# Optimization experiments

Hardware: AMD Instinct MI355X
Metric: run time of the kernel (lower is better)

## Reference

```python
import jax, jax.numpy as jnp
import numpy as np

B, T, D = 1, 4096, 1024
H, DK, DV, L = 16, 64, 64, 32
ROT_SCALE = 1.0  # rotary_pos_scale default


def _rotate_half(x):
    # '... (j d) -> ... j d' with j=2, then cat((-x2, x1))
    x1, x2 = jnp.split(x, 2, axis=-1)
    return jnp.concatenate((-x2, x1), axis=-1)


def _apply_rope(freqs, x, scale):
    # freqs: [T, L] broadcasts over leading dims of x [..., T, L]
    return x * jnp.cos(freqs) * scale + _rotate_half(x) * jnp.sin(freqs) * scale


def setup_inputs() -> dict:
    key = jax.random.key(0)
    ks = jax.random.split(key, 9)
    q = jax.random.normal(ks[0], (B, T, D), jnp.float32)
    k = jax.random.normal(ks[1], (B, T, D), jnp.float32)
    v = jax.random.normal(ks[2], (B, T, D), jnp.float32)
    mask = jnp.tril(jnp.ones((T, T), dtype=bool))  # causal [T, T]
    rotary_freqs = jax.random.normal(ks[3], (T, L), jnp.float32)
    s = 0.02
    w_q = jax.random.normal(ks[4], (H * DK, D), jnp.float32) * s
    w_k = jax.random.normal(ks[5], (H * DK, D), jnp.float32) * s
    w_v = jax.random.normal(ks[6], (H * DV, D), jnp.float32) * s
    w_o = jax.random.normal(ks[7], (D, H * DV), jnp.float32) * s
    return {"q": q, "k": k, "v": v, "mask": mask, "rotary_freqs": rotary_freqs,
            "w_q": w_q, "w_k": w_k, "w_v": w_v, "w_o": w_o}


def reference(q, k, v, mask, rotary_freqs, w_q, w_k, w_v, w_o):
    # project and split heads: '... T (H k) -> ... H T k'
    def heads(x, w, dh):
        y = jnp.einsum('btd,ed->bte', x, w)
        return y.reshape(B, T, H, dh).transpose(0, 2, 1, 3)  # [B,H,T,dh]

    q_i = heads(q, w_q, DK)
    k_i = heads(k, w_k, DK)
    v_i = heads(v, w_v, DV)

    # rotary pos emb on first L dims of q, k AND v (unusual: v too)
    q_scale, k_scale = ROT_SCALE, ROT_SCALE ** (-1.0)

    def rope(x, scale):
        xl, xr = x[..., :L], x[..., L:]
        return jnp.concatenate((_apply_rope(rotary_freqs, xl, scale), xr), axis=-1)

    q_i = rope(q_i, q_scale)
    k_i = rope(k_i, k_scale)
    v_i = rope(v_i, k_scale)

    s_qk = jnp.einsum('bhik,bhjk->bhij', q_i, k_i) / (DK ** 0.5)
    neg = -jnp.finfo(s_qk.dtype).max
    s_qk = jnp.where(mask, s_qk, neg)  # mask broadcasts [T,T] -> [B,H,T,T]
    attn = jax.nn.softmax(s_qk, axis=-1)
    vals = jnp.einsum('bhij,bhjv->bhiv', attn, v_i)
    vals = vals.transpose(0, 2, 1, 3).reshape(B, T, H * DV)  # '... H T v -> ... T (H v)'
    out = jnp.einsum('bte,oe->bto', vals, w_o)
    return out
```

## Files before the change

### kernel.cpp

```cpp
#include <hip/hip_runtime.h>

typedef unsigned short u16;
typedef unsigned int u32;
typedef short bf16x8 __attribute__((ext_vector_type(8)));
typedef float f32x4 __attribute__((ext_vector_type(4)));
typedef unsigned short u16x4 __attribute__((ext_vector_type(4)));
typedef unsigned short u16x8 __attribute__((ext_vector_type(8)));

__device__ __forceinline__ u16 f32_to_bf16(float f) {
    u32 u = __float_as_uint(f);
    u += 0x7FFFu + ((u >> 16) & 1u);
    return (u16)(u >> 16);
}
__device__ __forceinline__ short f32_to_bf16_trunc(float f) {
    return (short)(__float_as_uint(f) >> 16);
}

__device__ __forceinline__ void gl_lds16(const u16* g, u16* l) {
    __builtin_amdgcn_global_load_lds(
        (const __attribute__((address_space(1))) u32*)g,
        (__attribute__((address_space(3))) u32*)l, 16, 0, 0);
}

struct CastArgs {
    const float* src[7];
    u16* dst[7];
    int n4[7];
};

__global__ __launch_bounds__(256) void cast_kernel(CastArgs a) {
    const int y = blockIdx.y;
    const float* s = a.src[y];
    u16* d = a.dst[y];
    const int n4 = a.n4[y];
    for (int i = blockIdx.x * blockDim.x + threadIdx.x; i < n4; i += gridDim.x * blockDim.x) {
        f32x4 v = *(const f32x4*)&s[(size_t)i * 4];
        u16x4 o = { f32_to_bf16(v[0]), f32_to_bf16(v[1]), f32_to_bf16(v[2]), f32_to_bf16(v[3]) };
        *(u16x4*)&d[(size_t)i * 4] = o;
    }
}

#define GK 1024
#define GN 1024
#define GM 4096

__global__ __launch_bounds__(256) void gemm_rope(
    const u16* __restrict__ A0, const u16* __restrict__ A1, const u16* __restrict__ A2,
    const u16* __restrict__ W0, const u16* __restrict__ W1, const u16* __restrict__ W2,
    u16* __restrict__ C0, u16* __restrict__ C1, u16* __restrict__ C2,
    const float* __restrict__ freqs)
{
    __shared__ u16 SM[8192];
    u16* As = SM;
    u16* Bs = SM + 4096;

    const int z = blockIdx.z;
    const u16* A = (z == 0) ? A0 : ((z == 1) ? A1 : A2);
    const u16* W = (z == 0) ? W0 : ((z == 1) ? W1 : W2);
    u16* Cb      = (z == 0) ? C0 : ((z == 1) ? C1 : C2);
    const float ascale = (z == 0) ? 0.125f : 1.0f;

    const int tid  = threadIdx.x;
    const int w    = tid >> 6;
    const int lane = tid & 63;
    const int quad = lane >> 4;
    const int l16  = lane & 15;
    const int m0 = blockIdx.x * 128;
    const int n0 = blockIdx.y * 128;
    const int wm = (w >> 1) * 64;
    const int wn = (w & 1) * 64;

    const int sr = tid >> 2;
    const int sc = (tid & 3) * 8;
    const size_t aoff0 = (size_t)(m0 + sr) * GK + sc;
    const size_t aoff1 = aoff0 + (size_t)64 * GK;
    const size_t boff0 = (size_t)(n0 + sr) * GK + sc;
    const size_t boff1 = boff0 + (size_t)64 * GK;
    u16* ldsA0 = &As[w * 512];
    u16* ldsA1 = &As[2048 + w * 512];
    u16* ldsB0 = &Bs[w * 512];
    u16* ldsB1 = &Bs[2048 + w * 512];

    f32x4 acc[4][4];
    for (int i = 0; i < 4; i++)
        for (int j = 0; j < 4; j++) acc[i][j] = 0.f;

    for (int k0 = 0; k0 < GK; k0 += 32) {
        gl_lds16(A + aoff0 + k0, ldsA0);
        gl_lds16(A + aoff1 + k0, ldsA1);
        gl_lds16(W + boff0 + k0, ldsB0);
        gl_lds16(W + boff1 + k0, ldsB1);
        __syncthreads();

        bf16x8 af[4], bfr[4];
        for (int t = 0; t < 4; t++) {
            af[t]  = *(const bf16x8*)&As[(wm + t * 16 + l16) * 32 + quad * 8];
            bfr[t] = *(const bf16x8*)&Bs[(wn + t * 16 + l16) * 32 + quad * 8];
        }
        for (int mt = 0; mt < 4; mt++)
            for (int nt = 0; nt < 4; nt++)
                acc[mt][nt] = __builtin_amdgcn_mfma_f32_16x16x32_bf16(
                    af[mt], bfr[nt], acc[mt][nt], 0, 0, 0);
        __syncthreads();
    }
    u16* tr = SM + w * 1152;

    const int hh = (n0 + wn) >> 6;
    const size_t tb = (size_t)hh * 262144 + (size_t)((m0 + wm) >> 6) * 4096;

    if (z != 2) {
        for (int mt = 0; mt < 4; mt++) {
            #pragma unroll
            for (int r = 0; r < 4; r++) {
                int m = m0 + wm + mt * 16 + quad * 4 + r;
                float v0 = acc[mt][0][r];
                float v1 = acc[mt][1][r];
                float f0 = freqs[m * 32 + l16];
                float f1 = freqs[m * 32 + 16 + l16];
                float s0, c0, s1, c1;
                __sincosf(f0, &s0, &c0);
                __sincosf(f1, &s1, &c1);
                int row = quad * 4 + r;
                tr[row * 72 + l16]      = f32_to_bf16((v0 * c0 - v1 * s0) * ascale);
                tr[row * 72 + 16 + l16] = f32_to_bf16((v1 * c1 + v0 * s1) * ascale);
                tr[row * 72 + 32 + l16] = f32_to_bf16(acc[mt][2][r] * ascale);
                tr[row * 72 + 48 + l16] = f32_to_bf16(acc[mt][3][r] * ascale);
            }
            u16x8 va = *(const u16x8*)&tr[l16 * 72 + quad * 16];
            u16x8 vb = *(const u16x8*)&tr[l16 * 72 + quad * 16 + 8];
            if (z == 0) {
                size_t base = (size_t)(m0 + wm + mt * 16 + l16) * GN + n0 + wn + quad * 16;
                *(u16x8*)&Cb[base]     = va;
                *(u16x8*)&Cb[base + 8] = vb;
            } else {
                size_t base = tb + (size_t)(quad >> 1) * 2048
                            + (size_t)(mt * 16 + l16) * 32 + (quad & 1) * 16;
                *(u16x8*)&Cb[base]     = va;
                *(u16x8*)&Cb[base + 8] = vb;
            }
        }
    } else {
        for (int mt = 0; mt < 4; mt++) {
            float o0[4], o1[4];
            for (int r = 0; r < 4; r++) {
                int m = m0 + wm + mt * 16 + quad * 4 + r;
                float v0 = acc[mt][0][r];
                float v1 = acc[mt][1][r];
                float f0 = freqs[m * 32 + l16];
                float f1 = freqs[m * 32 + 16 + l16];
                float s0, c0, s1, c1;
                __sincosf(f0, &s0, &c0);
                __sincosf(f1, &s1, &c1);
                o0[r] = v0 * c0 - v1 * s0;
                o1[r] = v1 * c1 + v0 * s1;
            }
            const int ks = mt >> 1;
            const int sl = 4 * (mt & 1) + 8 * quad;
            const size_t hb = tb + (size_t)ks * 2048 + sl;
            u16x4 u;
            u = { f32_to_bf16(o0[0]), f32_to_bf16(o0[1]), f32_to_bf16(o0[2]), f32_to_bf16(o0[3]) };
            *(u16x4*)&Cb[hb + (size_t)l16 * 32] = u;
            u = { f32_to_bf16(o1[0]), f32_to_bf16(o1[1]), f32_to_bf16(o1[2]), f32_to_bf16(o1[3]) };
            *(u16x4*)&Cb[hb + (size_t)(16 + l16) * 32] = u;
            u = { f32_to_bf16(acc[mt][2][0]), f32_to_bf16(acc[mt][2][1]),
                  f32_to_bf16(acc[mt][2][2]), f32_to_bf16(acc[mt][2][3]) };
            *(u16x4*)&Cb[hb + (size_t)(32 + l16) * 32] = u;
            u = { f32_to_bf16(acc[mt][3][0]), f32_to_bf16(acc[mt][3][1]),
                  f32_to_bf16(acc[mt][3][2]), f32_to_bf16(acc[mt][3][3]) };
            *(u16x4*)&Cb[hb + (size_t)(48 + l16) * 32] = u;
        }
    }
}

__global__ __launch_bounds__(256) void gemm_out(
    const u16* __restrict__ A, const u16* __restrict__ W,
    float* __restrict__ O0, float* __restrict__ O1)
{
    __shared__ u16 SM[8704];
    u16* As = SM;
    u16* Bs = SM + 4096;

    const int z = blockIdx.z;
    float* C = z ? O1 : O0;
    const int kbeg = z * 512;

    const int tid  = threadIdx.x;
    const int w    = tid >> 6;
    const int lane = tid & 63;
    const int quad = lane >> 4;
    const int l16  = lane & 15;
    const int m0 = blockIdx.x * 128;
    const int n0 = blockIdx.y * 128;
    const int wm = (w >> 1) * 64;
    const int wn = (w & 1) * 64;

    const int sr = tid >> 2;
    const int sc = (tid & 3) * 8;
    const size_t aoff0 = (size_t)(m0 + sr) * GK + kbeg + sc;
    const size_t aoff1 = aoff0 + (size_t)64 * GK;
    const size_t boff0 = (size_t)(n0 + sr) * GK + kbeg + sc;
    const size_t boff1 = boff0 + (size_t)64 * GK;
    u16* ldsA0 = &As[w * 512];
    u16* ldsA1 = &As[2048 + w * 512];
    u16* ldsB0 = &Bs[w * 512];
    u16* ldsB1 = &Bs[2048 + w * 512];

    f32x4 acc[4][4];
    for (int i = 0; i < 4; i++)
        for (int j = 0; j < 4; j++) acc[i][j] = 0.f;

    for (int k0 = 0; k0 < 512; k0 += 32) {
        gl_lds16(A + aoff0 + k0, ldsA0);
        gl_lds16(A + aoff1 + k0, ldsA1);
        gl_lds16(W + boff0 + k0, ldsB0);
        gl_lds16(W + boff1 + k0, ldsB1);
        __syncthreads();

        bf16x8 af[4], bfr[4];
        for (int t = 0; t < 4; t++) {
            af[t]  = *(const bf16x8*)&As[(wm + t * 16 + l16) * 32 + quad * 8];
            bfr[t] = *(const bf16x8*)&Bs[(wn + t * 16 + l16) * 32 + quad * 8];
        }
        for (int mt = 0; mt < 4; mt++)
            for (int nt = 0; nt < 4; nt++)
                acc[mt][nt] = __builtin_amdgcn_mfma_f32_16x16x32_bf16(
                    af[mt], bfr[nt], acc[mt][nt], 0, 0, 0);
        __syncthreads();
    }

    float* tr = (float*)SM + w * 1088;
    for (int mt = 0; mt < 4; mt++) {
        #pragma unroll
        for (int nt = 0; nt < 4; nt++)
            #pragma unroll
            for (int r = 0; r < 4; r++)
                tr[(quad * 4 + r) * 68 + nt * 16 + l16] = acc[mt][nt][r];
        size_t base = (size_t)(m0 + wm + mt * 16 + l16) * GN + n0 + wn + quad * 16;
        #pragma unroll
        for (int c = 0; c < 4; c++) {
            f32x4 v = *(const f32x4*)&tr[l16 * 68 + quad * 16 + c * 4];
            *(f32x4*)&C[base + c * 4] = v;
        }
    }
}

__global__ __launch_bounds__(256) void add_kernel(
    const float* __restrict__ O0, const float* __restrict__ O1, float* __restrict__ out)
{
    int i = blockIdx.x * 256 + threadIdx.x;
    f32x4 a = *(const f32x4*)&O0[(size_t)i * 4];
    f32x4 b = *(const f32x4*)&O1[(size_t)i * 4];
    f32x4 c = a + b;
    *(f32x4*)&out[(size_t)i * 4] = c;
}

__global__ __launch_bounds__(256) void attn_kernel(
    const u16* __restrict__ Qb, const u16* __restrict__ KT,
    const u16* __restrict__ VTg, u16* __restrict__ valsb)
{
    __shared__ u16 KV[2][8192];
    __shared__ float Ow[4][16 * 68];

    const int tid  = threadIdx.x;
    const int w    = tid >> 6;
    const int lane = tid & 63;
    const int quad = lane >> 4;
    const int l16  = lane & 15;
    const int HD = 1024;

    const int id = blockIdx.x;
    const int h  = (id & 7) * 2 + ((id >> 3) & 1);
    const int p  = id >> 4;

    const u16* kt = KT  + (size_t)h * 262144;
    const u16* vt = VTg + (size_t)h * 262144;

    for (int gi = 0; gi < 2; gi++) {
        const int qb = gi ? (63 - p) : p;

        const size_t qrow = (size_t)(qb * 64 + w * 16 + l16);
        bf16x8 bq0 = *(const bf16x8*)&Qb[qrow * HD + h * 64 + quad * 8];
        bf16x8 bq1 = *(const bf16x8*)&Qb[qrow * HD + h * 64 + 32 + quad * 8];

        f32x4 o[4];
        #pragma unroll
        for (int i = 0; i < 4; i++) o[i] = 0.f;
        float lsum = 0.f;
        const int q_local = w * 16 + l16;

        __syncthreads();
        {
            const u16* ksrc = kt;  const u16* vsrc = vt;
            #pragma unroll
            for (int i = 0; i < 2; i++) {
                gl_lds16(ksrc + i * 2048 + w * 512 + (lane & 63) * 8, &KV[0][i * 2048 + w * 512]);
                gl_lds16(vsrc + i * 2048 + w * 512 + (lane & 63) * 8, &KV[0][4096 + i * 2048 + w * 512]);
            }
        }

        for (int kb = 0; kb <= qb; kb++) {
            __syncthreads();
            if (kb < qb) {
                const int nb = (kb + 1) & 1;
                const u16* ksrc = kt + (size_t)(kb + 1) * 4096;
                const u16* vsrc = vt + (size_t)(kb + 1) * 4096;
                #pragma unroll
                for (int i = 0; i < 2; i++) {
                    gl_lds16(ksrc + i * 2048 + w * 512 + lane * 8, &KV[nb][i * 2048 + w * 512]);
                    gl_lds16(vsrc + i * 2048 + w * 512 + lane * 8, &KV[nb][4096 + i * 2048 + w * 512]);
                }
            }
            const u16* Ksb = &KV[kb & 1][0];
            const u16* Vsb = &KV[kb & 1][4096];

            f32x4 s[4];
            #pragma unroll
            for (int nt2 = 0; nt2 < 4; nt2++) {
                bf16x8 ak0 = *(const bf16x8*)&Ksb[(nt2 * 16 + l16) * 32 + quad * 8];
                bf16x8 ak1 = *(const bf16x8*)&Ksb[2048 + (nt2 * 16 + l16) * 32 + quad * 8];
                f32x4 z4 = { 0.f, 0.f, 0.f, 0.f };
                s[nt2] = __builtin_amdgcn_mfma_f32_16x16x32_bf16(ak0, bq0, z4, 0, 0, 0);
                s[nt2] = __builtin_amdgcn_mfma_f32_16x16x32_bf16(ak1, bq1, s[nt2], 0, 0, 0);
            }

            if (kb == qb) {
                #pragma unroll
                for (int nt2 = 0; nt2 < 4; nt2++)
                    #pragma unroll
                    for (int r = 0; r < 4; r++)
                        if (nt2 * 16 + quad * 4 + r > q_local) s[nt2][r] = -1e30f;
            }

            bf16x8 av[8];
            #pragma unroll
            for (int nv = 0; nv < 4; nv++) {
                av[nv * 2]     = *(const bf16x8*)&Vsb[(nv * 16 + l16) * 32 + quad * 8];
                av[nv * 2 + 1] = *(const bf16x8*)&Vsb[2048 + (nv * 16 + l16) * 32 + quad * 8];
            }

            #pragma unroll
            for (int nt2 = 0; nt2 < 4; nt2++)
                #pragma unroll
                for (int r = 0; r < 4; r++) {
                    float pe = __expf(s[nt2][r] - 16.f);
                    s[nt2][r] = pe;
                    lsum += pe;
                }

            bf16x8 bp0 = { f32_to_bf16_trunc(s[0][0]), f32_to_bf16_trunc(s[0][1]),
                           f32_to_bf16_trunc(s[0][2]), f32_to_bf16_trunc(s[0][3]),
                           f32_to_bf16_trunc(s[1][0]), f32_to_bf16_trunc(s[1][1]),
                           f32_to_bf16_trunc(s[1][2]), f32_to_bf16_trunc(s[1][3]) };
            bf16x8 bp1 = { f32_to_bf16_trunc(s[2][0]), f32_to_bf16_trunc(s[2][1]),
                           f32_to_bf16_trunc(s[2][2]), f32_to_bf16_trunc(s[2][3]),
                           f32_to_bf16_trunc(s[3][0]), f32_to_bf16_trunc(s[3][1]),
                           f32_to_bf16_trunc(s[3][2]), f32_to_bf16_trunc(s[3][3]) };
            #pragma unroll
            for (int nv = 0; nv < 4; nv++) {
                o[nv] = __builtin_amdgcn_mfma_f32_16x16x32_bf16(av[nv * 2], bp0, o[nv], 0, 0, 0);
                o[nv] = __builtin_amdgcn_mfma_f32_16x16x32_bf16(av[nv * 2 + 1], bp1, o[nv], 0, 0, 0);
            }
        }

        lsum += __shfl_xor(lsum, 16);
        lsum += __shfl_xor(lsum, 32);
        const float inv = 1.f / lsum;
        float* myOw = Ow[w];
        #pragma unroll
        for (int nv = 0; nv < 4; nv++)
            #pragma unroll
            for (int r = 0; r < 4; r++)
                myOw[l16 * 68 + nv * 16 + quad * 4 + r] = o[nv][r] * inv;
        #pragma unroll
        for (int i = 0; i < 4; i++) {
            int row = i * 4 + quad;
            f32x4 vv = *(const f32x4*)&myOw[row * 68 + l16 * 4];
            u16x4 u = { f32_to_bf16(vv[0]), f32_to_bf16(vv[1]), f32_to_bf16(vv[2]), f32_to_bf16(vv[3]) };
            *(u16x4*)&valsb[(size_t)(qb * 64 + w * 16 + row) * HD + h * 64 + l16 * 4] = u;
        }
    }
}

extern "C" void kernel_launch(void* const* d_in, const int* in_sizes, int n_in,
                              void* d_out, int out_size, void* d_ws, size_t ws_size,
                              hipStream_t stream) {
    const float* q     = (const float*)d_in[0];
    const float* k     = (const float*)d_in[1];
    const float* v     = (const float*)d_in[2];
    const float* freqs = (const float*)d_in[4];
    const float* wq    = (const float*)d_in[5];
    const float* wk    = (const float*)d_in[6];
    const float* wv    = (const float*)d_in[7];
    const float* wo    = (const float*)d_in[8];

    u16* B = (u16*)d_ws;
    u16* qc  = B;
    u16* kc  = B + (size_t)4194304;
    u16* vc  = B + (size_t)8388608;
    u16* wqc = B + (size_t)12582912;
    u16* wkc = B + (size_t)13631488;
    u16* wvc = B + (size_t)14680064;
    u16* woc = B + (size_t)15728640;
    u16* Qb  = B + (size_t)16777216;
    u16* KT  = B + (size_t)20971520;
    u16* VT  = B + (size_t)25165824;
    u16* valsb = qc;
    float* O0 = (float*)(B + (size_t)16777216);
    float* O1 = (float*)(B + (size_t)25165824);

    CastArgs ca;
    ca.src[0] = q;  ca.dst[0] = qc;  ca.n4[0] = 1048576;
    ca.src[1] = k;  ca.dst[1] = kc;  ca.n4[1] = 1048576;
    ca.src[2] = v;  ca.dst[2] = vc;  ca.n4[2] = 1048576;
    ca.src[3] = wq; ca.dst[3] = wqc; ca.n4[3] = 262144;
    ca.src[4] = wk; ca.dst[4] = wkc; ca.n4[4] = 262144;
    ca.src[5] = wv; ca.dst[5] = wvc; ca.n4[5] = 262144;
    ca.src[6] = wo; ca.dst[6] = woc; ca.n4[6] = 262144;
    cast_kernel<<<dim3(1024, 7), 256, 0, stream>>>(ca);

    gemm_rope<<<dim3(32, 8, 3), 256, 0, stream>>>(
        qc, kc, vc, wqc, wkc, wvc, Qb, KT, VT, freqs);

    attn_kernel<<<dim3(512), 256, 0, stream>>>(Qb, KT, VT, valsb);

    gemm_out<<<dim3(32, 8, 2), 256, 0, stream>>>(valsb, woc, O0, O1);

    add_kernel<<<dim3(4096), 256, 0, stream>>>(O0, O1, (float*)d_out);
}
```

Measured before the change: 286.4 us.

## Rework attention to 128-query blocks per workgroup and drop split-K output GEMM

The attention kernel now gives each workgroup one 128-row query block, with each wave handling 32 query rows as two 16-row tiles. This replaces the earlier scheme of two 64-row blocks processed one after the other, so every K/V tile loaded into LDS serves twice as many queries. Blocks are paired light and heavy to balance the causal work, waves stop early past their diagonal, and launch bounds now request 2 blocks per CU. The output projection drops the split-K path, the fp32 partial buffers and the add kernel. It computes 64x128 tiles over the full K range and writes straight to the output, at the cost of a longer serial K loop per block and more registers per wave in attention.

```diff
diff --git a/kernel.cpp b/kernel.cpp
--- a/kernel.cpp
+++ b/kernel.cpp
@@ -173,55 +173,45 @@
 }
 
 __global__ __launch_bounds__(256) void gemm_out(
-    const u16* __restrict__ A, const u16* __restrict__ W,
-    float* __restrict__ O0, float* __restrict__ O1)
+    const u16* __restrict__ A, const u16* __restrict__ W, float* __restrict__ C)
 {
     __shared__ u16 SM[8704];
     u16* As = SM;
-    u16* Bs = SM + 4096;
-
-    const int z = blockIdx.z;
-    float* C = z ? O1 : O0;
-    const int kbeg = z * 512;
+    u16* Bs = SM + 2048;
 
     const int tid  = threadIdx.x;
     const int w    = tid >> 6;
     const int lane = tid & 63;
     const int quad = lane >> 4;
     const int l16  = lane & 15;
-    const int m0 = blockIdx.x * 128;
+    const int m0 = blockIdx.x * 64;
     const int n0 = blockIdx.y * 128;
-    const int wm = (w >> 1) * 64;
+    const int wm = (w >> 1) * 32;
     const int wn = (w & 1) * 64;
 
-    const int sr = tid >> 2;
-    const int sc = (tid & 3) * 8;
-    const size_t aoff0 = (size_t)(m0 + sr) * GK + kbeg + sc;
-    const size_t aoff1 = aoff0 + (size_t)64 * GK;
-    const size_t boff0 = (size_t)(n0 + sr) * GK + kbeg + sc;
+    const size_t aoff  = (size_t)(m0 + (tid >> 2)) * GK + (tid & 3) * 8;
+    const size_t boff0 = (size_t)(n0 + (tid >> 2)) * GK + (tid & 3) * 8;
     const size_t boff1 = boff0 + (size_t)64 * GK;
-    u16* ldsA0 = &As[w * 512];
-    u16* ldsA1 = &As[2048 + w * 512];
+    u16* ldsA  = &As[w * 512];
     u16* ldsB0 = &Bs[w * 512];
     u16* ldsB1 = &Bs[2048 + w * 512];
 
-    f32x4 acc[4][4];
-    for (int i = 0; i < 4; i++)
+    f32x4 acc[2][4];
+    for (int i = 0; i < 2; i++)
         for (int j = 0; j < 4; j++) acc[i][j] = 0.f;
 
-    for (int k0 = 0; k0 < 512; k0 += 32) {
-        gl_lds16(A + aoff0 + k0, ldsA0);
-        gl_lds16(A + aoff1 + k0, ldsA1);
+    for (int k0 = 0; k0 < GK; k0 += 32) {
+        gl_lds16(A + aoff + k0, ldsA);
         gl_lds16(W + boff0 + k0, ldsB0);
         gl_lds16(W + boff1 + k0, ldsB1);
         __syncthreads();
 
-        bf16x8 af[4], bfr[4];
-        for (int t = 0; t < 4; t++) {
-            af[t]  = *(const bf16x8*)&As[(wm + t * 16 + l16) * 32 + quad * 8];
+        bf16x8 af[2], bfr[4];
+        for (int t = 0; t < 2; t++)
+            af[t] = *(const bf16x8*)&As[(wm + t * 16 + l16) * 32 + quad * 8];
+        for (int t = 0; t < 4; t++)
             bfr[t] = *(const bf16x8*)&Bs[(wn + t * 16 + l16) * 32 + quad * 8];
-        }
-        for (int mt = 0; mt < 4; mt++)
+        for (int mt = 0; mt < 2; mt++)
             for (int nt = 0; nt < 4; nt++)
                 acc[mt][nt] = __builtin_amdgcn_mfma_f32_16x16x32_bf16(
                     af[mt], bfr[nt], acc[mt][nt], 0, 0, 0);
@@ -229,7 +219,7 @@
     }
 
     float* tr = (float*)SM + w * 1088;
-    for (int mt = 0; mt < 4; mt++) {
+    for (int mt = 0; mt < 2; mt++) {
         #pragma unroll
         for (int nt = 0; nt < 4; nt++)
             #pragma unroll
@@ -244,22 +234,12 @@
     }
 }
 
-__global__ __launch_bounds__(256) void add_kernel(
-    const float* __restrict__ O0, const float* __restrict__ O1, float* __restrict__ out)
-{
-    int i = blockIdx.x * 256 + threadIdx.x;
-    f32x4 a = *(const f32x4*)&O0[(size_t)i * 4];
-    f32x4 b = *(const f32x4*)&O1[(size_t)i * 4];
-    f32x4 c = a + b;
-    *(f32x4*)&out[(size_t)i * 4] = c;
-}
-
-__global__ __launch_bounds__(256) void attn_kernel(
+__global__ __launch_bounds__(256, 2) void attn_kernel(
     const u16* __restrict__ Qb, const u16* __restrict__ KT,
     const u16* __restrict__ VTg, u16* __restrict__ valsb)
 {
     __shared__ u16 KV[2][8192];
-    __shared__ float Ow[4][16 * 68];
+    __shared__ float Ow[4][32 * 68];
 
     const int tid  = threadIdx.x;
     const int w    = tid >> 6;
@@ -268,116 +248,139 @@
     const int l16  = lane & 15;
     const int HD = 1024;
 
-    const int id = blockIdx.x;
-    const int h  = (id & 7) * 2 + ((id >> 3) & 1);
-    const int p  = id >> 4;
+    const int id  = blockIdx.x;
+    const int h   = (id & 7) * 2 + ((id >> 3) & 1);
+    const int idx = id >> 4;
+    const int g   = (idx & 1) ? (31 - (idx >> 1)) : (idx >> 1);
 
     const u16* kt = KT  + (size_t)h * 262144;
     const u16* vt = VTg + (size_t)h * 262144;
 
-    for (int gi = 0; gi < 2; gi++) {
-        const int qb = gi ? (63 - p) : p;
-
-        const size_t qrow = (size_t)(qb * 64 + w * 16 + l16);
-        bf16x8 bq0 = *(const bf16x8*)&Qb[qrow * HD + h * 64 + quad * 8];
-        bf16x8 bq1 = *(const bf16x8*)&Qb[qrow * HD + h * 64 + 32 + quad * 8];
-
-        f32x4 o[4];
-        #pragma unroll
-        for (int i = 0; i < 4; i++) o[i] = 0.f;
-        float lsum = 0.f;
-        const int q_local = w * 16 + l16;
-
+    const int kb_end  = 2 * g + 1;
+    const int kb_diag = 2 * g + (w >> 1);
+    const int qbase   = (w & 1) * 32;
+
+    bf16x8 bq[2][2];
+    #pragma unroll
+    for (int qt = 0; qt < 2; qt++)
+        #pragma unroll
+        for (int ks = 0; ks < 2; ks++)
+            bq[qt][ks] = *(const bf16x8*)&Qb[(size_t)(128 * g + 32 * w + qt * 16 + l16) * HD
+                                             + h * 64 + ks * 32 + quad * 8];
+
+    f32x4 o[2][4];
+    #pragma unroll
+    for (int qt = 0; qt < 2; qt++)
+        #pragma unroll
+        for (int nv = 0; nv < 4; nv++) o[qt][nv] = 0.f;
+    float lsum[2] = { 0.f, 0.f };
+
+    #pragma unroll
+    for (int i = 0; i < 2; i++) {
+        gl_lds16(kt + i * 2048 + w * 512 + lane * 8, &KV[0][i * 2048 + w * 512]);
+        gl_lds16(vt + i * 2048 + w * 512 + lane * 8, &KV[0][4096 + i * 2048 + w * 512]);
+    }
+
+    for (int kb = 0; kb <= kb_end; kb++) {
         __syncthreads();
-        {
-            const u16* ksrc = kt;  const u16* vsrc = vt;
+        if (kb < kb_end) {
+            const int nb = (kb + 1) & 1;
+            const u16* ksrc = kt + (size_t)(kb + 1) * 4096;
+            const u16* vsrc = vt + (size_t)(kb + 1) * 4096;
             #pragma unroll
             for (int i = 0; i < 2; i++) {
-                gl_lds16(ksrc + i * 2048 + w * 512 + (lane & 63) * 8, &KV[0][i * 2048 + w * 512]);
-                gl_lds16(vsrc + i * 2048 + w * 512 + (lane & 63) * 8, &KV[0][4096 + i * 2048 + w * 512]);
-            }
-        }
-
-        for (int kb = 0; kb <= qb; kb++) {
-            __syncthreads();
-            if (kb < qb) {
-                const int nb = (kb + 1) & 1;
-                const u16* ksrc = kt + (size_t)(kb + 1) * 4096;
-                const u16* vsrc = vt + (size_t)(kb + 1) * 4096;
+                gl_lds16(ksrc + i * 2048 + w * 512 + lane * 8, &KV[nb][i * 2048 + w * 512]);
+                gl_lds16(vsrc + i * 2048 + w * 512 + lane * 8, &KV[nb][4096 + i * 2048 + w * 512]);
+            }
+        }
+        if (kb > kb_diag) continue;
+
+        const u16* Ksb = &KV[kb & 1][0];
+        const u16* Vsb = &KV[kb & 1][4096];
+
+        f32x4 s[2][4];
+        #pragma unroll
+        for (int nt = 0; nt < 4; nt++) {
+            bf16x8 ak0 = *(const bf16x8*)&Ksb[(nt * 16 + l16) * 32 + quad * 8];
+            bf16x8 ak1 = *(const bf16x8*)&Ksb[2048 + (nt * 16 + l16) * 32 + quad * 8];
+            #pragma unroll
+            for (int qt = 0; qt < 2; qt++) {
+                f32x4 z4 = { 0.f, 0.f, 0.f, 0.f };
+                s[qt][nt] = __builtin_amdgcn_mfma_f32_16x16x32_bf16(ak0, bq[qt][0], z4, 0, 0, 0);
+                s[qt][nt] = __builtin_amdgcn_mfma_f32_16x16x32_bf16(ak1, bq[qt][1], s[qt][nt], 0, 0, 0);
+            }
+        }
+
+        if (kb == kb_diag) {
+            #pragma unroll
+            for (int qt = 0; qt < 2; qt++) {
+                const int ql = qbase + qt * 16 + l16;
                 #pragma unroll
-                for (int i = 0; i < 2; i++) {
-                    gl_lds16(ksrc + i * 2048 + w * 512 + lane * 8, &KV[nb][i * 2048 + w * 512]);
-                    gl_lds16(vsrc + i * 2048 + w * 512 + lane * 8, &KV[nb][4096 + i * 2048 + w * 512]);
-                }
-            }
-            const u16* Ksb = &KV[kb & 1][0];
-            const u16* Vsb = &KV[kb & 1][4096];
-
-            f32x4 s[4];
-            #pragma unroll
-            for (int nt2 = 0; nt2 < 4; nt2++) {
-                bf16x8 ak0 = *(const bf16x8*)&Ksb[(nt2 * 16 + l16) * 32 + quad * 8];
-                bf16x8 ak1 = *(const bf16x8*)&Ksb[2048 + (nt2 * 16 + l16) * 32 + quad * 8];
-                f32x4 z4 = { 0.f, 0.f, 0.f, 0.f };
-                s[nt2] = __builtin_amdgcn_mfma_f32_16x16x32_bf16(ak0, bq0, z4, 0, 0, 0);
-                s[nt2] = __builtin_amdgcn_mfma_f32_16x16x32_bf16(ak1, bq1, s[nt2], 0, 0, 0);
-            }
-
-            if (kb == qb) {
-                #pragma unroll
-                for (int nt2 = 0; nt2 < 4; nt2++)
+                for (int nt = 0; nt < 4; nt++)
                     #pragma unroll
                     for (int r = 0; r < 4; r++)
-                        if (nt2 * 16 + quad * 4 + r > q_local) s[nt2][r] = -1e30f;
-            }
-
-            bf16x8 av[8];
-            #pragma unroll
-            for (int nv = 0; nv < 4; nv++) {
-                av[nv * 2]     = *(const bf16x8*)&Vsb[(nv * 16 + l16) * 32 + quad * 8];
-                av[nv * 2 + 1] = *(const bf16x8*)&Vsb[2048 + (nv * 16 + l16) * 32 + quad * 8];
-            }
-
-            #pragma unroll
-            for (int nt2 = 0; nt2 < 4; nt2++)
+                        if (nt * 16 + quad * 4 + r > ql) s[qt][nt][r] = -1e30f;
+            }
+        }
+
+        bf16x8 av[8];
+        #pragma unroll
+        for (int nv = 0; nv < 4; nv++) {
+            av[nv * 2]     = *(const bf16x8*)&Vsb[(nv * 16 + l16) * 32 + quad * 8];
+            av[nv * 2 + 1] = *(const bf16x8*)&Vsb[2048 + (nv * 16 + l16) * 32 + quad * 8];
+        }
+
+        #pragma unroll
+        for (int qt = 0; qt < 2; qt++) {
+            float ls = 0.f;
+            #pragma unroll
+            for (int nt = 0; nt < 4; nt++)
                 #pragma unroll
                 for (int r = 0; r < 4; r++) {
-                    float pe = __expf(s[nt2][r] - 16.f);
-                    s[nt2][r] = pe;
-                    lsum += pe;
+                    float pe = __expf(s[qt][nt][r] - 16.f);
+                    s[qt][nt][r] = pe;
+                    ls += pe;
                 }
-
-            bf16x8 bp0 = { f32_to_bf16_trunc(s[0][0]), f32_to_bf16_trunc(s[0][1]),
-                           f32_to_bf16_trunc(s[0][2]), f32_to_bf16_trunc(s[0][3]),
-                           f32_to_bf16_trunc(s[1][0]), f32_to_bf16_trunc(s[1][1]),
-                           f32_to_bf16_trunc(s[1][2]), f32_to_bf16_trunc(s[1][3]) };
-            bf16x8 bp1 = { f32_to_bf16_trunc(s[2][0]), f32_to_bf16_trunc(s[2][1]),
-                           f32_to_bf16_trunc(s[2][2]), f32_to_bf16_trunc(s[2][3]),
-                           f32_to_bf16_trunc(s[3][0]), f32_to_bf16_trunc(s[3][1]),
-                           f32_to_bf16_trunc(s[3][2]), f32_to_bf16_trunc(s[3][3]) };
+            lsum[qt] += ls;
+
+            bf16x8 bp0 = { f32_to_bf16_trunc(s[qt][0][0]), f32_to_bf16_trunc(s[qt][0][1]),
+                           f32_to_bf16_trunc(s[qt][0][2]), f32_to_bf16_trunc(s[qt][0][3]),
+                           f32_to_bf16_trunc(s[qt][1][0]), f32_to_bf16_trunc(s[qt][1][1]),
+                           f32_to_bf16_trunc(s[qt][1][2]), f32_to_bf16_trunc(s[qt][1][3]) };
+            bf16x8 bp1 = { f32_to_bf16_trunc(s[qt][2][0]), f32_to_bf16_trunc(s[qt][2][1]),
+                           f32_to_bf16_trunc(s[qt][2][2]), f32_to_bf16_trunc(s[qt][2][3]),
+                           f32_to_bf16_trunc(s[qt][3][0]), f32_to_bf16_trunc(s[qt][3][1]),
+                           f32_to_bf16_trunc(s[qt][3][2]), f32_to_bf16_trunc(s[qt][3][3]) };
             #pragma unroll
             for (int nv = 0; nv < 4; nv++) {
-                o[nv] = __builtin_amdgcn_mfma_f32_16x16x32_bf16(av[nv * 2], bp0, o[nv], 0, 0, 0);
-                o[nv] = __builtin_amdgcn_mfma_f32_16x16x32_bf16(av[nv * 2 + 1], bp1, o[nv], 0, 0, 0);
-            }
-        }
-
-        lsum += __shfl_xor(lsum, 16);
-        lsum += __shfl_xor(lsum, 32);
-        const float inv = 1.f / lsum;
-        float* myOw = Ow[w];
+                o[qt][nv] = __builtin_amdgcn_mfma_f32_16x16x32_bf16(av[nv * 2], bp0, o[qt][nv], 0, 0, 0);
+                o[qt][nv] = __builtin_amdgcn_mfma_f32_16x16x32_bf16(av[nv * 2 + 1], bp1, o[qt][nv], 0, 0, 0);
+            }
+        }
+    }
+
+    float linv[2];
+    #pragma unroll
+    for (int qt = 0; qt < 2; qt++) {
+        float ls = lsum[qt];
+        ls += __shfl_xor(ls, 16);
+        ls += __shfl_xor(ls, 32);
+        linv[qt] = 1.f / ls;
+    }
+    float* myOw = Ow[w];
+    #pragma unroll
+    for (int qt = 0; qt < 2; qt++)
         #pragma unroll
         for (int nv = 0; nv < 4; nv++)
             #pragma unroll
             for (int r = 0; r < 4; r++)
-                myOw[l16 * 68 + nv * 16 + quad * 4 + r] = o[nv][r] * inv;
-        #pragma unroll
-        for (int i = 0; i < 4; i++) {
-            int row = i * 4 + quad;
-            f32x4 vv = *(const f32x4*)&myOw[row * 68 + l16 * 4];
-            u16x4 u = { f32_to_bf16(vv[0]), f32_to_bf16(vv[1]), f32_to_bf16(vv[2]), f32_to_bf16(vv[3]) };
-            *(u16x4*)&valsb[(size_t)(qb * 64 + w * 16 + row) * HD + h * 64 + l16 * 4] = u;
-        }
+                myOw[(qt * 16 + l16) * 68 + nv * 16 + quad * 4 + r] = o[qt][nv][r] * linv[qt];
+    #pragma unroll
+    for (int i = 0; i < 8; i++) {
+        int row = i * 4 + quad;
+        f32x4 vv = *(const f32x4*)&myOw[row * 68 + l16 * 4];
+        u16x4 u = { f32_to_bf16(vv[0]), f32_to_bf16(vv[1]), f32_to_bf16(vv[2]), f32_to_bf16(vv[3]) };
+        *(u16x4*)&valsb[(size_t)(128 * g + 32 * w + row) * HD + h * 64 + l16 * 4] = u;
     }
 }
 
@@ -405,8 +408,6 @@
     u16* KT  = B + (size_t)20971520;
     u16* VT  = B + (size_t)25165824;
     u16* valsb = qc;
-    float* O0 = (float*)(B + (size_t)16777216);
-    float* O1 = (float*)(B + (size_t)25165824);
 
     CastArgs ca;
     ca.src[0] = q;  ca.dst[0] = qc;  ca.n4[0] = 1048576;
@@ -423,7 +424,5 @@
 
     attn_kernel<<<dim3(512), 256, 0, stream>>>(Qb, KT, VT, valsb);
 
-    gemm_out<<<dim3(32, 8, 2), 256, 0, stream>>>(valsb, woc, O0, O1);
-
-    add_kernel<<<dim3(4096), 256, 0, stream>>>(O0, O1, (float*)d_out);
-}
+    gemm_out<<<dim3(64, 8), 256, 0, stream>>>(valsb, woc, (float*)d_out);
+}
```

Measured after the change: 289.6 us. Within noise of the previous version (+1.1%).

## Swizzle LDS tiles and drop split-K output GEMM plus add kernel

Applied to the files above, without the earlier changes.

Applies an XOR swizzle to the LDS layout in the projection GEMM, the attention K/V tiles and the output GEMM so that the bf16x8 fragment reads spread across banks instead of conflicting. The output GEMM stops splitting K into two partial buffers followed by a separate add kernel. It now uses 64x128 tiles over the full K and writes straight to the output, which removes one launch and the fp32 partial round-trip. The attention kernel also gets a launch-bounds occupancy hint of 2, which may limit the registers available to it.

```diff
diff --git a/kernel.cpp b/kernel.cpp
--- a/kernel.cpp
+++ b/kernel.cpp
@@ -21,6 +21,7 @@
         (const __attribute__((address_space(1))) u32*)g,
         (__attribute__((address_space(3))) u32*)l, 16, 0, 0);
 }
+
 
 struct CastArgs {
     const float* src[7];
@@ -71,7 +72,7 @@
     const int wn = (w & 1) * 64;
 
     const int sr = tid >> 2;
-    const int sc = (tid & 3) * 8;
+    const int sc = (((tid & 3) ^ ((tid >> 3) & 3))) * 8;
     const size_t aoff0 = (size_t)(m0 + sr) * GK + sc;
     const size_t aoff1 = aoff0 + (size_t)64 * GK;
     const size_t boff0 = (size_t)(n0 + sr) * GK + sc;
@@ -81,6 +82,8 @@
     u16* ldsB0 = &Bs[w * 512];
     u16* ldsB1 = &Bs[2048 + w * 512];
 
+    const int csw = (quad ^ ((l16 >> 1) & 3)) * 8;
+
     f32x4 acc[4][4];
     for (int i = 0; i < 4; i++)
         for (int j = 0; j < 4; j++) acc[i][j] = 0.f;
@@ -94,8 +97,8 @@
 
         bf16x8 af[4], bfr[4];
         for (int t = 0; t < 4; t++) {
-            af[t]  = *(const bf16x8*)&As[(wm + t * 16 + l16) * 32 + quad * 8];
-            bfr[t] = *(const bf16x8*)&Bs[(wn + t * 16 + l16) * 32 + quad * 8];
+            af[t]  = *(const bf16x8*)&As[(wm + t * 16 + l16) * 32 + csw];
+            bfr[t] = *(const bf16x8*)&Bs[(wn + t * 16 + l16) * 32 + csw];
         }
         for (int mt = 0; mt < 4; mt++)
             for (int nt = 0; nt < 4; nt++)
@@ -173,55 +176,49 @@
 }
 
 __global__ __launch_bounds__(256) void gemm_out(
-    const u16* __restrict__ A, const u16* __restrict__ W,
-    float* __restrict__ O0, float* __restrict__ O1)
+    const u16* __restrict__ A, const u16* __restrict__ W, float* __restrict__ C)
 {
     __shared__ u16 SM[8704];
     u16* As = SM;
-    u16* Bs = SM + 4096;
-
-    const int z = blockIdx.z;
-    float* C = z ? O1 : O0;
-    const int kbeg = z * 512;
+    u16* Bs = SM + 2048;
 
     const int tid  = threadIdx.x;
     const int w    = tid >> 6;
     const int lane = tid & 63;
     const int quad = lane >> 4;
     const int l16  = lane & 15;
-    const int m0 = blockIdx.x * 128;
+    const int m0 = blockIdx.x * 64;
     const int n0 = blockIdx.y * 128;
-    const int wm = (w >> 1) * 64;
+    const int wm = (w >> 1) * 32;
     const int wn = (w & 1) * 64;
 
     const int sr = tid >> 2;
-    const int sc = (tid & 3) * 8;
-    const size_t aoff0 = (size_t)(m0 + sr) * GK + kbeg + sc;
-    const size_t aoff1 = aoff0 + (size_t)64 * GK;
-    const size_t boff0 = (size_t)(n0 + sr) * GK + kbeg + sc;
+    const int sc = (((tid & 3) ^ ((tid >> 3) & 3))) * 8;
+    const size_t aoff  = (size_t)(m0 + sr) * GK + sc;
+    const size_t boff0 = (size_t)(n0 + sr) * GK + sc;
     const size_t boff1 = boff0 + (size_t)64 * GK;
-    u16* ldsA0 = &As[w * 512];
-    u16* ldsA1 = &As[2048 + w * 512];
+    u16* ldsA  = &As[w * 512];
     u16* ldsB0 = &Bs[w * 512];
     u16* ldsB1 = &Bs[2048 + w * 512];
 
-    f32x4 acc[4][4];
-    for (int i = 0; i < 4; i++)
+    const int csw = (quad ^ ((l16 >> 1) & 3)) * 8;
+
+    f32x4 acc[2][4];
+    for (int i = 0; i < 2; i++)
         for (int j = 0; j < 4; j++) acc[i][j] = 0.f;
 
-    for (int k0 = 0; k0 < 512; k0 += 32) {
-        gl_lds16(A + aoff0 + k0, ldsA0);
-        gl_lds16(A + aoff1 + k0, ldsA1);
+    for (int k0 = 0; k0 < GK; k0 += 32) {
+        gl_lds16(A + aoff + k0, ldsA);
         gl_lds16(W + boff0 + k0, ldsB0);
         gl_lds16(W + boff1 + k0, ldsB1);
         __syncthreads();
 
-        bf16x8 af[4], bfr[4];
-        for (int t = 0; t < 4; t++) {
-            af[t]  = *(const bf16x8*)&As[(wm + t * 16 + l16) * 32 + quad * 8];
-            bfr[t] = *(const bf16x8*)&Bs[(wn + t * 16 + l16) * 32 + quad * 8];
-        }
-        for (int mt = 0; mt < 4; mt++)
+        bf16x8 af[2], bfr[4];
+        for (int t = 0; t < 2; t++)
+            af[t] = *(const bf16x8*)&As[(wm + t * 16 + l16) * 32 + csw];
+        for (int t = 0; t < 4; t++)
+            bfr[t] = *(const bf16x8*)&Bs[(wn + t * 16 + l16) * 32 + csw];
+        for (int mt = 0; mt < 2; mt++)
             for (int nt = 0; nt < 4; nt++)
                 acc[mt][nt] = __builtin_amdgcn_mfma_f32_16x16x32_bf16(
                     af[mt], bfr[nt], acc[mt][nt], 0, 0, 0);
@@ -229,7 +226,7 @@
     }
 
     float* tr = (float*)SM + w * 1088;
-    for (int mt = 0; mt < 4; mt++) {
+    for (int mt = 0; mt < 2; mt++) {
         #pragma unroll
         for (int nt = 0; nt < 4; nt++)
             #pragma unroll
@@ -244,17 +241,7 @@
     }
 }
 
-__global__ __launch_bounds__(256) void add_kernel(
-    const float* __restrict__ O0, const float* __restrict__ O1, float* __restrict__ out)
-{
-    int i = blockIdx.x * 256 + threadIdx.x;
-    f32x4 a = *(const f32x4*)&O0[(size_t)i * 4];
-    f32x4 b = *(const f32x4*)&O1[(size_t)i * 4];
-    f32x4 c = a + b;
-    *(f32x4*)&out[(size_t)i * 4] = c;
-}
-
-__global__ __launch_bounds__(256) void attn_kernel(
+__global__ __launch_bounds__(256, 2) void attn_kernel(
     const u16* __restrict__ Qb, const u16* __restrict__ KT,
     const u16* __restrict__ VTg, u16* __restrict__ valsb)
 {
@@ -275,6 +262,9 @@
     const u16* kt = KT  + (size_t)h * 262144;
     const u16* vt = VTg + (size_t)h * 262144;
 
+    const int dmaoff = (lane >> 2) * 32 + ((lane & 3) ^ ((lane >> 3) & 3)) * 8;
+    const int csw = (quad ^ ((l16 >> 1) & 3)) * 8;
+
     for (int gi = 0; gi < 2; gi++) {
         const int qb = gi ? (63 - p) : p;
 
@@ -289,13 +279,10 @@
         const int q_local = w * 16 + l16;
 
         __syncthreads();
-        {
-            const u16* ksrc = kt;  const u16* vsrc = vt;
-            #pragma unroll
-            for (int i = 0; i < 2; i++) {
-                gl_lds16(ksrc + i * 2048 + w * 512 + (lane & 63) * 8, &KV[0][i * 2048 + w * 512]);
-                gl_lds16(vsrc + i * 2048 + w * 512 + (lane & 63) * 8, &KV[0][4096 + i * 2048 + w * 512]);
-            }
+        #pragma unroll
+        for (int i = 0; i < 2; i++) {
+            gl_lds16(kt + i * 2048 + w * 512 + dmaoff, &KV[0][i * 2048 + w * 512]);
+            gl_lds16(vt + i * 2048 + w * 512 + dmaoff, &KV[0][4096 + i * 2048 + w * 512]);
         }
 
         for (int kb = 0; kb <= qb; kb++) {
@@ -306,8 +293,8 @@
                 const u16* vsrc = vt + (size_t)(kb + 1) * 4096;
                 #pragma unroll
                 for (int i = 0; i < 2; i++) {
-                    gl_lds16(ksrc + i * 2048 + w * 512 + lane * 8, &KV[nb][i * 2048 + w * 512]);
-                    gl_lds16(vsrc + i * 2048 + w * 512 + lane * 8, &KV[nb][4096 + i * 2048 + w * 512]);
+                    gl_lds16(ksrc + i * 2048 + w * 512 + dmaoff, &KV[nb][i * 2048 + w * 512]);
+                    gl_lds16(vsrc + i * 2048 + w * 512 + dmaoff, &KV[nb][4096 + i * 2048 + w * 512]);
                 }
             }
             const u16* Ksb = &KV[kb & 1][0];
@@ -316,8 +303,8 @@
             f32x4 s[4];
             #pragma unroll
             for (int nt2 = 0; nt2 < 4; nt2++) {
-                bf16x8 ak0 = *(const bf16x8*)&Ksb[(nt2 * 16 + l16) * 32 + quad * 8];
-                bf16x8 ak1 = *(const bf16x8*)&Ksb[2048 + (nt2 * 16 + l16) * 32 + quad * 8];
+                bf16x8 ak0 = *(const bf16x8*)&Ksb[(nt2 * 16 + l16) * 32 + csw];
+                bf16x8 ak1 = *(const bf16x8*)&Ksb[2048 + (nt2 * 16 + l16) * 32 + csw];
                 f32x4 z4 = { 0.f, 0.f, 0.f, 0.f };
                 s[nt2] = __builtin_amdgcn_mfma_f32_16x16x32_bf16(ak0, bq0, z4, 0, 0, 0);
                 s[nt2] = __builtin_amdgcn_mfma_f32_16x16x32_bf16(ak1, bq1, s[nt2], 0, 0, 0);
@@ -334,8 +321,8 @@
             bf16x8 av[8];
             #pragma unroll
             for (int nv = 0; nv < 4; nv++) {
-                av[nv * 2]     = *(const bf16x8*)&Vsb[(nv * 16 + l16) * 32 + quad * 8];
-                av[nv * 2 + 1] = *(const bf16x8*)&Vsb[2048 + (nv * 16 + l16) * 32 + quad * 8];
+                av[nv * 2]     = *(const bf16x8*)&Vsb[(nv * 16 + l16) * 32 + csw];
+                av[nv * 2 + 1] = *(const bf16x8*)&Vsb[2048 + (nv * 16 + l16) * 32 + csw];
             }
 
             #pragma unroll
@@ -405,8 +392,6 @@
     u16* KT  = B + (size_t)20971520;
     u16* VT  = B + (size_t)25165824;
     u16* valsb = qc;
-    float* O0 = (float*)(B + (size_t)16777216);
-    float* O1 = (float*)(B + (size_t)25165824);
 
     CastArgs ca;
     ca.src[0] = q;  ca.dst[0] = qc;  ca.n4[0] = 1048576;
@@ -423,7 +408,5 @@
 
     attn_kernel<<<dim3(512), 256, 0, stream>>>(Qb, KT, VT, valsb);
 
-    gemm_out<<<dim3(32, 8, 2), 256, 0, stream>>>(valsb, woc, O0, O1);
-
-    add_kernel<<<dim3(4096), 256, 0, stream>>>(O0, O1, (float*)d_out);
-}
+    gemm_out<<<dim3(64, 8), 256, 0, stream>>>(valsb, woc, (float*)d_out);
+}
```

After: 272.2 us. -5.0%, faster.
